# Performance work log

Measured on AMD Instinct MI355X. Metric: run time of the kernel, lower is better.

## Reference

```python
import jax, jax.numpy as jnp
import numpy as np

B, T, D = 2, 2048, 2048
H, HD = 32, 64  # n_heads, head_dim; H*HD == attn_dim == D


def _rope(x, cos, sin):
    # x: (B,T,H,HD) with interleaved (real, imag) pairs on last dim
    b, t, h, hd = x.shape
    x2 = x.reshape(b, t, h, hd // 2, 2)
    xr, xi = x2[..., 0], x2[..., 1]
    c = cos[None, :, None, :]  # (1,T,1,HD/2)
    s = sin[None, :, None, :]
    out_r = xr * c - xi * s
    out_i = xr * s + xi * c
    return jnp.stack([out_r, out_i], axis=-1).reshape(b, t, h, hd)


def setup_inputs() -> dict:
    key = jax.random.key(0)
    ks = jax.random.split(key, 5)
    x = jax.random.normal(ks[0], (B, T, D), dtype=jnp.float32)
    scale = 0.02
    wq = jax.random.normal(ks[1], (D, D), dtype=jnp.float32) * scale
    wk = jax.random.normal(ks[2], (D, D), dtype=jnp.float32) * scale
    wv = jax.random.normal(ks[3], (D, D), dtype=jnp.float32) * scale
    wo = jax.random.normal(ks[4], (D, D), dtype=jnp.float32) * scale
    # standard RoPE frequencies, theta = 10000
    inv_freq = 1.0 / (10000.0 ** (jnp.arange(0, HD, 2, dtype=jnp.float32) / HD))  # (HD/2,)
    angles = jnp.arange(T, dtype=jnp.float32)[:, None] * inv_freq[None, :]  # (T, HD/2)
    return {
        "x": x,
        "freqs_cos": jnp.cos(angles),
        "freqs_sin": jnp.sin(angles),
        "wq": wq, "wk": wk, "wv": wv, "wo": wo,
    }


def reference(x, freqs_cos, freqs_sin, wq, wk, wv, wo):
    b, t, d = x.shape
    # fused-style QKV projections (nn.Linear: x @ W.T, no bias)
    q = (x @ wq.T).reshape(b, t, H, HD)
    k = (x @ wk.T).reshape(b, t, H, HD)
    v = (x @ wv.T).reshape(b, t, H, HD)
    q = _rope(q, freqs_cos, freqs_sin)
    k = _rope(k, freqs_cos, freqs_sin)
    # causal SDPA, scale = 1/sqrt(head_dim)
    scale = 1.0 / jnp.sqrt(jnp.float32(HD))
    scores = jnp.einsum("bqhd,bkhd->bhqk", q, k) * scale  # (B,H,T,T)
    causal = jnp.tril(jnp.ones((t, t), dtype=bool))
    scores = jnp.where(causal[None, None], scores, jnp.float32(-jnp.inf))
    attn = jax.nn.softmax(scores, axis=-1)
    y = jnp.einsum("bhqk,bkhd->bqhd", attn, v).reshape(b, t, H * HD)
    return y @ wo.T
```

## Files before the change

### kernel.cpp

```cpp
#include <hip/hip_runtime.h>
#include <hip/hip_bf16.h>
#include <stdint.h>


typedef __bf16 bf16_t;
typedef __bf16 bf16x4 __attribute__((ext_vector_type(4)));
typedef __bf16 bf16x8 __attribute__((ext_vector_type(8)));
typedef float  f32x4  __attribute__((ext_vector_type(4)));

constexpr int B_ = 2, T_ = 2048, D_ = 2048, H_ = 32, HD_ = 64;
constexpr int M_ = B_ * T_;

__device__ __forceinline__ void async_copy16(const bf16_t* g, bf16_t* l) {
  __builtin_amdgcn_global_load_lds(
      (const __attribute__((address_space(1))) void*)g,
      (__attribute__((address_space(3))) void*)l, 16, 0, 0);
}

__global__ __launch_bounds__(256) void cast_f32_bf16(
    const float* __restrict__ src, bf16_t* __restrict__ dst, int n4)
{
  const int i = blockIdx.x * 256 + threadIdx.x;
  if (i >= n4) return;
  const float4 v = ((const float4*)src)[i];
  bf16x4 o;
  o[0] = (bf16_t)v.x; o[1] = (bf16_t)v.y; o[2] = (bf16_t)v.z; o[3] = (bf16_t)v.w;
  ((bf16x4*)dst)[i] = o;
}

template <typename OutT>
__global__ __launch_bounds__(256, 2) void gemm_bt(
    const bf16_t* __restrict__ A, const bf16_t* __restrict__ B,
    OutT* __restrict__ C, int M, int N, int K)
{
  __shared__ __attribute__((aligned(16))) bf16_t As[128 * 32];
  __shared__ __attribute__((aligned(16))) bf16_t Bs[128 * 32];

  const int tid    = threadIdx.x;
  const int w      = tid >> 6;
  const int l      = tid & 63;
  const int quad   = l >> 4;
  const int lane16 = l & 15;
  const int bm0 = blockIdx.x * 128;
  const int bn0 = blockIdx.y * 128;
  const int wm  = (w >> 1) * 64;
  const int wn  = (w & 1) * 64;
  const int srow = l >> 2;
  const int scol = (l & 3) * 8;

  const bf16_t* Ag = A + (size_t)bm0 * K;
  const bf16_t* Bg = B + (size_t)bn0 * K;

  f32x4 acc[4][4] = {};

  for (int kk = 0; kk < K; kk += 32) {
    __syncthreads();
#pragma unroll
    for (int s0 = 0; s0 < 2; ++s0) {
      const int s = w + s0 * 4;
      async_copy16(Ag + (size_t)(s * 16 + srow) * K + kk + scol, &As[s * 512]);
      async_copy16(Bg + (size_t)(s * 16 + srow) * K + kk + scol, &Bs[s * 512]);
    }
    __syncthreads();

    bf16x8 af[4], bfr[4];
#pragma unroll
    for (int i = 0; i < 4; ++i)
      af[i] = *(const bf16x8*)&As[(wm + i * 16 + lane16) * 32 + quad * 8];
#pragma unroll
    for (int j = 0; j < 4; ++j)
      bfr[j] = *(const bf16x8*)&Bs[(wn + j * 16 + lane16) * 32 + quad * 8];
#pragma unroll
    for (int i = 0; i < 4; ++i)
#pragma unroll
      for (int j = 0; j < 4; ++j)
        acc[i][j] = __builtin_amdgcn_mfma_f32_16x16x32_bf16(af[i], bfr[j],
                                                            acc[i][j], 0, 0, 0);
  }

#pragma unroll
  for (int i = 0; i < 4; ++i) {
#pragma unroll
    for (int r = 0; r < 4; ++r) {
      const size_t row = (size_t)(bm0 + wm + i * 16 + quad * 4 + r);
#pragma unroll
      for (int j = 0; j < 4; ++j) {
        const int col = bn0 + wn + j * 16 + lane16;
        C[row * N + col] = (OutT)acc[i][j][r];
      }
    }
  }
}

__global__ __launch_bounds__(256, 2) void gemm_qkv(
    const bf16_t* __restrict__ A, const bf16_t* __restrict__ B,
    bf16_t* __restrict__ Cq, bf16_t* __restrict__ Ck, bf16_t* __restrict__ Cv,
    int M, int K)
{
  __shared__ __attribute__((aligned(16))) bf16_t As[128 * 32];
  __shared__ __attribute__((aligned(16))) bf16_t Bs[128 * 32];

  const int tid    = threadIdx.x;
  const int w      = tid >> 6;
  const int l      = tid & 63;
  const int quad   = l >> 4;
  const int lane16 = l & 15;
  const int bm0 = blockIdx.x * 128;
  const int bn0 = blockIdx.y * 128;
  const int wm  = (w >> 1) * 64;
  const int wn  = (w & 1) * 64;
  const int srow = l >> 2;
  const int scol = (l & 3) * 8;

  const bf16_t* Ag = A + (size_t)bm0 * K;
  const bf16_t* Bg = B + (size_t)bn0 * K;

  f32x4 acc[4][4] = {};

  for (int kk = 0; kk < K; kk += 32) {
    __syncthreads();
#pragma unroll
    for (int s0 = 0; s0 < 2; ++s0) {
      const int s = w + s0 * 4;
      async_copy16(Ag + (size_t)(s * 16 + srow) * K + kk + scol, &As[s * 512]);
      async_copy16(Bg + (size_t)(s * 16 + srow) * K + kk + scol, &Bs[s * 512]);
    }
    __syncthreads();

    bf16x8 af[4], bfr[4];
#pragma unroll
    for (int i = 0; i < 4; ++i)
      af[i] = *(const bf16x8*)&As[(wm + i * 16 + lane16) * 32 + quad * 8];
#pragma unroll
    for (int j = 0; j < 4; ++j)
      bfr[j] = *(const bf16x8*)&Bs[(wn + j * 16 + lane16) * 32 + quad * 8];
#pragma unroll
    for (int i = 0; i < 4; ++i)
#pragma unroll
      for (int j = 0; j < 4; ++j)
        acc[i][j] = __builtin_amdgcn_mfma_f32_16x16x32_bf16(af[i], bfr[j],
                                                            acc[i][j], 0, 0, 0);
  }

  bf16_t* Cb = (bn0 < 2048) ? Cq : (bn0 < 4096) ? Ck : Cv;
  const int cb0 = (bn0 & 2047) + wn;
#pragma unroll
  for (int i = 0; i < 4; ++i) {
#pragma unroll
    for (int r = 0; r < 4; ++r) {
      const size_t row = (size_t)(bm0 + wm + i * 16 + quad * 4 + r);
#pragma unroll
      for (int j = 0; j < 4; ++j)
        Cb[row * 2048 + cb0 + j * 16 + lane16] = (bf16_t)acc[i][j][r];
    }
  }
}

__global__ __launch_bounds__(256) void rope_kernel(
    bf16_t* __restrict__ q, bf16_t* __restrict__ k,
    const float* __restrict__ cosb, const float* __restrict__ sinb, int npair)
{
  const int idx = blockIdx.x * 256 + threadIdx.x;
  if (idx >= npair) return;
  const int p = idx & 31;
  const int t = (idx >> 10) & (T_ - 1);
  const float c = cosb[t * 32 + p];
  const float s = sinb[t * 32 + p];
  const size_t off = (size_t)idx * 2;

  const float qr = (float)q[off], qi = (float)q[off + 1];
  q[off]     = (bf16_t)((qr * c - qi * s) * 0.125f);
  q[off + 1] = (bf16_t)((qr * s + qi * c) * 0.125f);

  const float kr = (float)k[off], ki = (float)k[off + 1];
  k[off]     = (bf16_t)(kr * c - ki * s);
  k[off + 1] = (bf16_t)(kr * s + ki * c);
}

__global__ __launch_bounds__(256, 2) void flash_attn(
    const bf16_t* __restrict__ Q, const bf16_t* __restrict__ K,
    const bf16_t* __restrict__ V, bf16_t* __restrict__ Y)
{
  __shared__ __attribute__((aligned(16))) bf16_t Kf[4096];
  __shared__ __attribute__((aligned(16))) bf16_t Vf[4096];
  __shared__ __attribute__((aligned(16))) bf16_t Pt[4 * 2 * 16 * 68];

  const int tid    = threadIdx.x;
  const int w      = tid >> 6;
  const int l      = tid & 63;
  const int quad   = l >> 4;
  const int lane16 = l & 15;
  const int bh = blockIdx.y;
  const int b  = bh >> 5;
  const int h  = bh & 31;
  const int gx = blockIdx.x;
  int qa[2];
  qa[0] = gx * 128 + w * 32;
  qa[1] = (15 - gx) * 128 + w * 32;
  const size_t rs = (size_t)H_ * HD_;

  const bf16_t* Qb = Q + ((size_t)b * T_) * rs + h * HD_;
  const bf16_t* Kb = K + ((size_t)b * T_) * rs + h * HD_;
  const bf16_t* Vb = V + ((size_t)b * T_) * rs + h * HD_;

  bf16x8 qf[2][2][2];
#pragma unroll
  for (int g = 0; g < 2; ++g)
#pragma unroll
    for (int t = 0; t < 2; ++t)
#pragma unroll
      for (int c = 0; c < 2; ++c)
        qf[g][t][c] = *(const bf16x8*)(Qb + (size_t)(qa[g] + t * 16 + lane16) * rs +
                                       c * 32 + quad * 8);

  f32x4 o[2][2][4] = {};
  float lsum[2][2] = {};

  const int koff = tid >> 3;
  const int oct  = tid & 7;
  const int d0   = oct * 8;
  const int kc = oct >> 2, kq = oct & 3;
  const int nV = oct >> 1, base16 = (oct & 1) * 8;

  bf16_t* const PtW = Pt + w * (2 * 16 * 68);

  const int nsteps = (15 - gx) * 2 + 2;

  bf16x8 kr[2], vr[2];
#pragma unroll
  for (int hf = 0; hf < 2; ++hf) {
    const int key = hf * 32 + koff;
    kr[hf] = *(const bf16x8*)(Kb + (size_t)key * rs + d0);
    vr[hf] = *(const bf16x8*)(Vb + (size_t)key * rs + d0);
  }

  for (int it = 0; it < nsteps; ++it) {
    const int k0 = it * 64;
    __syncthreads();
#pragma unroll
    for (int hf = 0; hf < 2; ++hf) {
      const int key = hf * 32 + koff;
      const int gK = ((kc * 4 + (key >> 4)) * 16 + (key & 15)) * 4 + kq;
      *(bf16x8*)&Kf[gK * 8] = kr[hf];
      const int cV = key >> 5, qV = (key >> 3) & 3, jV = key & 7;
#pragma unroll
      for (int i = 0; i < 8; ++i) {
        const int gv = ((cV * 4 + nV) * 16 + base16 + i) * 4 + qV;
        Vf[(gv ^ oct) * 8 + jV] = vr[hf][i];
      }
    }
    __syncthreads();
    if (it + 1 < nsteps) {
      const int k0n = k0 + 64;
#pragma unroll
      for (int hf = 0; hf < 2; ++hf) {
        const int key = k0n + hf * 32 + koff;
        kr[hf] = *(const bf16x8*)(Kb + (size_t)key * rs + d0);
        vr[hf] = *(const bf16x8*)(Vb + (size_t)key * rs + d0);
      }
    }

#pragma unroll
    for (int g = 0; g < 2; ++g) {
      if (k0 > qa[g] + 31) continue;

      f32x4 stx[4][2] = {};
#pragma unroll
      for (int c = 0; c < 2; ++c) {
#pragma unroll
        for (int kt = 0; kt < 4; ++kt) {
          const bf16x8 kfr =
              *(const bf16x8*)&Kf[(((c * 4 + kt) * 16 + lane16) * 4 + quad) * 8];
          stx[kt][0] = __builtin_amdgcn_mfma_f32_16x16x32_bf16(kfr, qf[g][0][c],
                                                               stx[kt][0], 0, 0, 0);
          stx[kt][1] = __builtin_amdgcn_mfma_f32_16x16x32_bf16(kfr, qf[g][1][c],
                                                               stx[kt][1], 0, 0, 0);
        }
      }

#pragma unroll
      for (int t = 0; t < 2; ++t) {
        const int qbase = qa[g] + t * 16;
#pragma unroll
        for (int kt = 0; kt < 4; ++kt) {
          const int kbase = k0 + kt * 16 + quad * 4;
          const bool anymask = (k0 + kt * 16 + 15) > qbase;
          float p[4];
#pragma unroll
          for (int r = 0; r < 4; ++r) {
            float s = stx[kt][t][r];
            if (anymask) s = (kbase + r > qbase + lane16) ? -1e30f : s;
            p[r] = __expf(s);
          }
          lsum[g][t] += (p[0] + p[1]) + (p[2] + p[3]);
          bf16x4 pv;
          pv[0] = (bf16_t)p[0]; pv[1] = (bf16_t)p[1];
          pv[2] = (bf16_t)p[2]; pv[3] = (bf16_t)p[3];
          *(bf16x4*)&PtW[(t * 16 + lane16) * 68 + kt * 16 + quad * 4] = pv;
        }
      }

#pragma unroll
      for (int c = 0; c < 2; ++c) {
        const bf16x8 pf0 = *(const bf16x8*)&PtW[(0 * 16 + lane16) * 68 + c * 32 + quad * 8];
        const bf16x8 pf1 = *(const bf16x8*)&PtW[(1 * 16 + lane16) * 68 + c * 32 + quad * 8];
#pragma unroll
        for (int n = 0; n < 4; ++n) {
          const int gv = ((c * 4 + n) * 16 + lane16) * 4 + quad;
          const int swz = n * 2 + (lane16 >> 3);
          const bf16x8 vfr = *(const bf16x8*)&Vf[(gv ^ swz) * 8];
          o[g][0][n] = __builtin_amdgcn_mfma_f32_16x16x32_bf16(pf0, vfr, o[g][0][n], 0, 0, 0);
          o[g][1][n] = __builtin_amdgcn_mfma_f32_16x16x32_bf16(pf1, vfr, o[g][1][n], 0, 0, 0);
        }
      }
    }
  }

  bf16_t* Yb = Y + ((size_t)b * T_) * rs + h * HD_;
#pragma unroll
  for (int g = 0; g < 2; ++g) {
#pragma unroll
    for (int t = 0; t < 2; ++t) {
      float lt = lsum[g][t];
      lt += __shfl_xor(lt, 16);
      lt += __shfl_xor(lt, 32);
#pragma unroll
      for (int r = 0; r < 4; ++r) {
        const float linv = 1.0f / __shfl(lt, quad * 4 + r);
        const size_t row = (size_t)(qa[g] + t * 16 + quad * 4 + r);
#pragma unroll
        for (int n = 0; n < 4; ++n)
          Yb[row * rs + n * 16 + lane16] = (bf16_t)(o[g][t][n][r] * linv);
      }
    }
  }
}

extern "C" void kernel_launch(void* const* d_in, const int* in_sizes, int n_in,
                              void* d_out, int out_size, void* d_ws, size_t ws_size,
                              hipStream_t stream)
{
  (void)in_sizes; (void)n_in; (void)out_size;
  const float* x  = (const float*)d_in[0];
  const float* fc = (const float*)d_in[1];
  const float* fs = (const float*)d_in[2];
  const float* wq = (const float*)d_in[3];
  const float* wk = (const float*)d_in[4];
  const float* wv = (const float*)d_in[5];
  const float* wo = (const float*)d_in[6];
  float* out = (float*)d_out;

  const size_t nx = (size_t)M_ * D_;
  const size_t nw = (size_t)D_ * D_;
  const dim3 blk(256);
  const int nx4 = (int)(nx / 4), nw4 = (int)(nw / 4);
  const dim3 gg(M_ / 128, D_ / 128);

  if (ws_size >= (3 * nw + 4 * nx) * sizeof(bf16_t)) {
    bf16_t* ws  = (bf16_t*)d_ws;
    bf16_t* wb3 = ws;
    bf16_t* xb  = ws + 3 * nw;
    bf16_t* qb  = xb + nx;
    bf16_t* kb  = qb + nx;
    bf16_t* vb  = kb + nx;
    bf16_t* yb  = xb;

    cast_f32_bf16<<<dim3(nx4 / 256), blk, 0, stream>>>(x, xb, nx4);
    cast_f32_bf16<<<dim3(nw4 / 256), blk, 0, stream>>>(wq, wb3, nw4);
    cast_f32_bf16<<<dim3(nw4 / 256), blk, 0, stream>>>(wk, wb3 + nw, nw4);
    cast_f32_bf16<<<dim3(nw4 / 256), blk, 0, stream>>>(wv, wb3 + 2 * nw, nw4);

    gemm_qkv<<<dim3(M_ / 128, 48), blk, 0, stream>>>(xb, wb3, qb, kb, vb, M_, D_);

    rope_kernel<<<dim3((B_ * T_ * H_ * 32) / 256), blk, 0, stream>>>(
        qb, kb, fc, fs, B_ * T_ * H_ * 32);
    flash_attn<<<dim3(8, B_ * H_), blk, 0, stream>>>(qb, kb, vb, yb);

    cast_f32_bf16<<<dim3(nw4 / 256), blk, 0, stream>>>(wo, wb3, nw4);
    gemm_bt<float><<<gg, blk, 0, stream>>>(yb, wb3, out, M_, D_, D_);
  } else {
    bf16_t* ws = (bf16_t*)d_ws;
    bf16_t* wb = ws;
    bf16_t* xb = ws + nw;
    bf16_t* qb = xb + nx;
    bf16_t* kb = qb + nx;
    bf16_t* vb = kb + nx;
    bf16_t* yb = xb;

    cast_f32_bf16<<<dim3(nx4 / 256), blk, 0, stream>>>(x, xb, nx4);
    cast_f32_bf16<<<dim3(nw4 / 256), blk, 0, stream>>>(wq, wb, nw4);
    gemm_bt<bf16_t><<<gg, blk, 0, stream>>>(xb, wb, qb, M_, D_, D_);
    cast_f32_bf16<<<dim3(nw4 / 256), blk, 0, stream>>>(wk, wb, nw4);
    gemm_bt<bf16_t><<<gg, blk, 0, stream>>>(xb, wb, kb, M_, D_, D_);
    cast_f32_bf16<<<dim3(nw4 / 256), blk, 0, stream>>>(wv, wb, nw4);
    gemm_bt<bf16_t><<<gg, blk, 0, stream>>>(xb, wb, vb, M_, D_, D_);

    rope_kernel<<<dim3((B_ * T_ * H_ * 32) / 256), blk, 0, stream>>>(
        qb, kb, fc, fs, B_ * T_ * H_ * 32);
    flash_attn<<<dim3(8, B_ * H_), blk, 0, stream>>>(qb, kb, vb, yb);

    cast_f32_bf16<<<dim3(nw4 / 256), blk, 0, stream>>>(wo, wb, nw4);
    gemm_bt<float><<<gg, blk, 0, stream>>>(yb, wb, out, M_, D_, D_);
  }
}
```

Before: 413.4 us.

## Pre-transpose V and load K/V MFMA fragments directly from global memory

Adds a kernel that transposes V per head into a (d, t) layout. The attention kernel then drops its shared-memory K/V staging and both block barriers, and each wave loads its MFMA operand fragments for K and transposed V straight from global memory. The log2(e) factor is folded into the Q scale so exp2f can replace __expf, and the grid is flattened so consecutive blocks are different heads. The trade-off is an extra transpose pass, and every wave now re-reads the same K/V tiles from global/L2 instead of sharing them through LDS, with no prefetch overlap.

```diff
diff --git a/kernel.cpp b/kernel.cpp
--- a/kernel.cpp
+++ b/kernel.cpp
@@ -167,22 +167,51 @@
   const float c = cosb[t * 32 + p];
   const float s = sinb[t * 32 + p];
   const size_t off = (size_t)idx * 2;
+  const float qs = 0.125f * 1.44269504f;
 
   const float qr = (float)q[off], qi = (float)q[off + 1];
-  q[off]     = (bf16_t)((qr * c - qi * s) * 0.125f);
-  q[off + 1] = (bf16_t)((qr * s + qi * c) * 0.125f);
+  q[off]     = (bf16_t)((qr * c - qi * s) * qs);
+  q[off + 1] = (bf16_t)((qr * s + qi * c) * qs);
 
   const float kr = (float)k[off], ki = (float)k[off + 1];
   k[off]     = (bf16_t)(kr * c - ki * s);
   k[off + 1] = (bf16_t)(kr * s + ki * c);
 }
 
+__global__ __launch_bounds__(256) void transpose_v(
+    const bf16_t* __restrict__ vb, bf16_t* __restrict__ vt)
+{
+  __shared__ __attribute__((aligned(16))) bf16_t Lt[64 * 72];
+  const int tid = threadIdx.x;
+  const int bh  = blockIdx.y;
+  const int tt  = blockIdx.x;
+  const int b   = bh >> 5, h = bh & 31;
+
+  const int tl = tid >> 3;
+  const int j8 = (tid & 7) * 8;
+
+#pragma unroll
+  for (int rep = 0; rep < 2; ++rep) {
+    const int t_loc = rep * 32 + tl;
+    const bf16x8 v = *(const bf16x8*)(vb + ((size_t)b * T_ + tt * 64 + t_loc) * 2048 +
+                                      h * 64 + j8);
+#pragma unroll
+    for (int i = 0; i < 8; ++i)
+      Lt[(j8 + i) * 72 + t_loc] = v[i];
+  }
+  __syncthreads();
+#pragma unroll
+  for (int rep = 0; rep < 2; ++rep) {
+    const int d = rep * 32 + tl;
+    const bf16x8 v = *(const bf16x8*)&Lt[d * 72 + j8];
+    *(bf16x8*)(vt + ((size_t)bh * 64 + d) * 2048 + tt * 64 + j8) = v;
+  }
+}
+
 __global__ __launch_bounds__(256, 2) void flash_attn(
     const bf16_t* __restrict__ Q, const bf16_t* __restrict__ K,
-    const bf16_t* __restrict__ V, bf16_t* __restrict__ Y)
-{
-  __shared__ __attribute__((aligned(16))) bf16_t Kf[4096];
-  __shared__ __attribute__((aligned(16))) bf16_t Vf[4096];
+    const bf16_t* __restrict__ Vt, bf16_t* __restrict__ Y)
+{
   __shared__ __attribute__((aligned(16))) bf16_t Pt[4 * 2 * 16 * 68];
 
   const int tid    = threadIdx.x;
@@ -190,18 +219,18 @@
   const int l      = tid & 63;
   const int quad   = l >> 4;
   const int lane16 = l & 15;
-  const int bh = blockIdx.y;
-  const int b  = bh >> 5;
-  const int h  = bh & 31;
-  const int gx = blockIdx.x;
+  const int bid = blockIdx.x;
+  const int gx  = bid >> 6;
+  const int bh  = bid & 63;
+  const int b   = bh >> 5, h = bh & 31;
   int qa[2];
   qa[0] = gx * 128 + w * 32;
   qa[1] = (15 - gx) * 128 + w * 32;
   const size_t rs = (size_t)H_ * HD_;
 
-  const bf16_t* Qb = Q + ((size_t)b * T_) * rs + h * HD_;
-  const bf16_t* Kb = K + ((size_t)b * T_) * rs + h * HD_;
-  const bf16_t* Vb = V + ((size_t)b * T_) * rs + h * HD_;
+  const bf16_t* Qb  = Q + ((size_t)b * T_) * rs + h * HD_;
+  const bf16_t* Kb  = K + ((size_t)b * T_) * rs + h * HD_;
+  const bf16_t* Vtb = Vt + (size_t)bh * HD_ * T_;
 
   bf16x8 qf[2][2][2];
 #pragma unroll
@@ -216,48 +245,23 @@
   f32x4 o[2][2][4] = {};
   float lsum[2][2] = {};
 
-  const int koff = tid >> 3;
-  const int oct  = tid & 7;
-  const int d0   = oct * 8;
-  const int kc = oct >> 2, kq = oct & 3;
-  const int nV = oct >> 1, base16 = (oct & 1) * 8;
-
   bf16_t* const PtW = Pt + w * (2 * 16 * 68);
-
   const int nsteps = (15 - gx) * 2 + 2;
-
-  bf16x8 kr[2], vr[2];
-#pragma unroll
-  for (int hf = 0; hf < 2; ++hf) {
-    const int key = hf * 32 + koff;
-    kr[hf] = *(const bf16x8*)(Kb + (size_t)key * rs + d0);
-    vr[hf] = *(const bf16x8*)(Vb + (size_t)key * rs + d0);
-  }
 
   for (int it = 0; it < nsteps; ++it) {
     const int k0 = it * 64;
-    __syncthreads();
-#pragma unroll
-    for (int hf = 0; hf < 2; ++hf) {
-      const int key = hf * 32 + koff;
-      const int gK = ((kc * 4 + (key >> 4)) * 16 + (key & 15)) * 4 + kq;
-      *(bf16x8*)&Kf[gK * 8] = kr[hf];
-      const int cV = key >> 5, qV = (key >> 3) & 3, jV = key & 7;
-#pragma unroll
-      for (int i = 0; i < 8; ++i) {
-        const int gv = ((cV * 4 + nV) * 16 + base16 + i) * 4 + qV;
-        Vf[(gv ^ oct) * 8 + jV] = vr[hf][i];
-      }
-    }
-    __syncthreads();
-    if (it + 1 < nsteps) {
-      const int k0n = k0 + 64;
-#pragma unroll
-      for (int hf = 0; hf < 2; ++hf) {
-        const int key = k0n + hf * 32 + koff;
-        kr[hf] = *(const bf16x8*)(Kb + (size_t)key * rs + d0);
-        vr[hf] = *(const bf16x8*)(Vb + (size_t)key * rs + d0);
-      }
+
+    bf16x8 kf[2][4], vf[2][4];
+#pragma unroll
+    for (int c = 0; c < 2; ++c) {
+#pragma unroll
+      for (int kt = 0; kt < 4; ++kt)
+        kf[c][kt] = *(const bf16x8*)(Kb + (size_t)(k0 + kt * 16 + lane16) * rs +
+                                     c * 32 + quad * 8);
+#pragma unroll
+      for (int n = 0; n < 4; ++n)
+        vf[c][n] = *(const bf16x8*)(Vtb + (size_t)(n * 16 + lane16) * T_ +
+                                    k0 + c * 32 + quad * 8);
     }
 
 #pragma unroll
@@ -269,11 +273,9 @@
       for (int c = 0; c < 2; ++c) {
 #pragma unroll
         for (int kt = 0; kt < 4; ++kt) {
-          const bf16x8 kfr =
-              *(const bf16x8*)&Kf[(((c * 4 + kt) * 16 + lane16) * 4 + quad) * 8];
-          stx[kt][0] = __builtin_amdgcn_mfma_f32_16x16x32_bf16(kfr, qf[g][0][c],
+          stx[kt][0] = __builtin_amdgcn_mfma_f32_16x16x32_bf16(kf[c][kt], qf[g][0][c],
                                                                stx[kt][0], 0, 0, 0);
-          stx[kt][1] = __builtin_amdgcn_mfma_f32_16x16x32_bf16(kfr, qf[g][1][c],
+          stx[kt][1] = __builtin_amdgcn_mfma_f32_16x16x32_bf16(kf[c][kt], qf[g][1][c],
                                                                stx[kt][1], 0, 0, 0);
         }
       }
@@ -290,7 +292,7 @@
           for (int r = 0; r < 4; ++r) {
             float s = stx[kt][t][r];
             if (anymask) s = (kbase + r > qbase + lane16) ? -1e30f : s;
-            p[r] = __expf(s);
+            p[r] = exp2f(s);
           }
           lsum[g][t] += (p[0] + p[1]) + (p[2] + p[3]);
           bf16x4 pv;
@@ -306,11 +308,8 @@
         const bf16x8 pf1 = *(const bf16x8*)&PtW[(1 * 16 + lane16) * 68 + c * 32 + quad * 8];
 #pragma unroll
         for (int n = 0; n < 4; ++n) {
-          const int gv = ((c * 4 + n) * 16 + lane16) * 4 + quad;
-          const int swz = n * 2 + (lane16 >> 3);
-          const bf16x8 vfr = *(const bf16x8*)&Vf[(gv ^ swz) * 8];
-          o[g][0][n] = __builtin_amdgcn_mfma_f32_16x16x32_bf16(pf0, vfr, o[g][0][n], 0, 0, 0);
-          o[g][1][n] = __builtin_amdgcn_mfma_f32_16x16x32_bf16(pf1, vfr, o[g][1][n], 0, 0, 0);
+          o[g][0][n] = __builtin_amdgcn_mfma_f32_16x16x32_bf16(pf0, vf[c][n], o[g][0][n], 0, 0, 0);
+          o[g][1][n] = __builtin_amdgcn_mfma_f32_16x16x32_bf16(pf1, vf[c][n], o[g][1][n], 0, 0, 0);
         }
       }
     }
@@ -355,6 +354,7 @@
   const dim3 blk(256);
   const int nx4 = (int)(nx / 4), nw4 = (int)(nw / 4);
   const dim3 gg(M_ / 128, D_ / 128);
+  const dim3 gt(T_ / 64, B_ * H_);
 
   if (ws_size >= (3 * nw + 4 * nx) * sizeof(bf16_t)) {
     bf16_t* ws  = (bf16_t*)d_ws;
@@ -363,7 +363,8 @@
     bf16_t* qb  = xb + nx;
     bf16_t* kb  = qb + nx;
     bf16_t* vb  = kb + nx;
-    bf16_t* yb  = xb;
+    bf16_t* vt  = xb;
+    bf16_t* yb  = vb;
 
     cast_f32_bf16<<<dim3(nx4 / 256), blk, 0, stream>>>(x, xb, nx4);
     cast_f32_bf16<<<dim3(nw4 / 256), blk, 0, stream>>>(wq, wb3, nw4);
@@ -374,7 +375,8 @@
 
     rope_kernel<<<dim3((B_ * T_ * H_ * 32) / 256), blk, 0, stream>>>(
         qb, kb, fc, fs, B_ * T_ * H_ * 32);
-    flash_attn<<<dim3(8, B_ * H_), blk, 0, stream>>>(qb, kb, vb, yb);
+    transpose_v<<<gt, blk, 0, stream>>>(vb, vt);
+    flash_attn<<<dim3(8 * B_ * H_), blk, 0, stream>>>(qb, kb, vt, yb);
 
     cast_f32_bf16<<<dim3(nw4 / 256), blk, 0, stream>>>(wo, wb3, nw4);
     gemm_bt<float><<<gg, blk, 0, stream>>>(yb, wb3, out, M_, D_, D_);
@@ -385,7 +387,8 @@
     bf16_t* qb = xb + nx;
     bf16_t* kb = qb + nx;
     bf16_t* vb = kb + nx;
-    bf16_t* yb = xb;
+    bf16_t* vt = xb;
+    bf16_t* yb = vb;
 
     cast_f32_bf16<<<dim3(nx4 / 256), blk, 0, stream>>>(x, xb, nx4);
     cast_f32_bf16<<<dim3(nw4 / 256), blk, 0, stream>>>(wq, wb, nw4);
@@ -397,7 +400,8 @@
 
     rope_kernel<<<dim3((B_ * T_ * H_ * 32) / 256), blk, 0, stream>>>(
         qb, kb, fc, fs, B_ * T_ * H_ * 32);
-    flash_attn<<<dim3(8, B_ * H_), blk, 0, stream>>>(qb, kb, vb, yb);
+    transpose_v<<<gt, blk, 0, stream>>>(vb, vt);
+    flash_attn<<<dim3(8 * B_ * H_), blk, 0, stream>>>(qb, kb, vt, yb);
 
     cast_f32_bf16<<<dim3(nw4 / 256), blk, 0, stream>>>(wo, wb, nw4);
     gemm_bt<float><<<gg, blk, 0, stream>>>(yb, wb, out, M_, D_, D_);
```

New measurement: 441.5 us. 6.8% more time.
